# Kernel optimization log

Measured on AMD Instinct MI355X. Metric: run time of the kernel, lower is better.

The kernel has to match this reference:

```python
import jax, jax.numpy as jnp
import numpy as np
from jax import lax

RADIUS = 4
SIGMA_1 = 5.0
SIGMA_2 = 1.0


def _gaussian_kernel_3d(radius, sigma):
    x = np.linspace(-radius, radius, 2 * radius + 1)
    xx, yy, zz = np.meshgrid(x, x, x)
    dist2 = xx ** 2 + yy ** 2 + zz ** 2
    k = np.exp(-dist2 / (2.0 * sigma ** 2)).astype(np.float32)
    return jnp.asarray(k)[None, None]  # [O=1, I=1, D, H, W]


def _conv3d_same(x, kernel, radius):
    # x: [B,1,D,H,W], kernel: [1,1,kd,kh,kw]
    pad = [(radius, radius)] * 3
    return lax.conv_general_dilated(
        x, kernel, window_strides=(1, 1, 1), padding=pad,
        dimension_numbers=('NCDHW', 'OIDHW', 'NCDHW'))


def setup_inputs() -> dict:
    key = jax.random.key(0)
    k1, k2 = jax.random.split(key)
    labels = jax.random.uniform(k1, (4, 1, 160, 160, 160), dtype=jnp.float32)
    inputs = jax.random.uniform(k2, (4, 1, 160, 160, 160), dtype=jnp.float32)
    return {"labels": labels, "inputs": inputs}


def reference(labels, inputs):
    kernel = _gaussian_kernel_3d(RADIUS, SIGMA_1)
    num_classes = 2
    p0 = labels[:, 0:1]  # [B,1,D,H,W]
    loss = jnp.float32(0.0)
    for k in range(num_classes):
        class_probs = p0 if k == 0 else 1.0 - p0
        class_mean = (jnp.mean(inputs * class_probs, axis=(2, 3, 4), keepdims=True)
                      / (jnp.mean(class_probs, axis=(2, 3, 4), keepdims=True) + 1e-5))
        diff = jnp.sum((inputs - class_mean) ** 2, axis=1, keepdims=True)  # [B,1,D,H,W]
        weights = jnp.exp(-(diff ** 2) / (SIGMA_2 ** 2))
        numerator = jnp.sum(class_probs * _conv3d_same(class_probs * weights, kernel, RADIUS))
        denominator = jnp.sum(class_probs * _conv3d_same(weights, kernel, RADIUS))
        # L1Loss(scalar, 0) == abs(scalar)
        loss = loss + jnp.abs(numerator / (denominator + 1e-6))
    return jnp.float32(num_classes) - loss
```

## Files before the change

kernel.cpp:

```cpp
#include <hip/hip_runtime.h>
#include <hip/hip_fp16.h>
#include <math.h>

#define NX   160
#define N2   25600
#define N3   4096000
#define NB   4

#define ZPB  2
#define NBLK_XY 8000
#define BLKS_PER_B 2000

#define ZCH  10
#define NBLK_Z 1600

#define SB_W 36
#define SB_PLANE (40 * SB_W)

__device__ __constant__ float G1[9] = {
    0.72614903f, 0.83527021f, 0.92311635f, 0.98019867f, 1.0f,
    0.98019867f, 0.92311635f, 0.83527021f, 0.72614903f};

#define ES_FULL 7.92946852f
__device__ __constant__ float ES_M[4] = {3.46473426f, 2.48453559f, 1.56141924f,
                                         0.72614903f};
__device__ inline float edge_sum(int i) {
    float s = ES_FULL;
    if (i < 4) s -= ES_M[i];
    if (i > NX - 5) s -= ES_M[NX - 1 - i];
    return s;
}

__device__ inline float4 f4_zero() { return make_float4(0.f, 0.f, 0.f, 0.f); }
__device__ inline float4 f4_axpy(float a, float4 b, float4 c) {
    return make_float4(c.x + a * b.x, c.y + a * b.y, c.z + a * b.z, c.w + a * b.w);
}

__device__ inline float4 load_t4(const __half* p) {
    uint2 u = *(const uint2*)p;
    __half2 a = *(const __half2*)&u.x;
    __half2 b = *(const __half2*)&u.y;
    float2 fa = __half22float2(a);
    float2 fb = __half22float2(b);
    return make_float4(fa.x, fa.y, fb.x, fb.y);
}

template <int NV>
__device__ inline void block_reduce_store(double* vals, double* dst) {
    __shared__ double red[4][NV];
    int lane = threadIdx.x & 63;
    int wave = threadIdx.x >> 6;
#pragma unroll
    for (int v = 0; v < NV; ++v) {
        double x = vals[v];
#pragma unroll
        for (int off = 32; off > 0; off >>= 1) x += __shfl_down(x, off, 64);
        if (lane == 0) red[wave][v] = x;
    }
    __syncthreads();
    if (threadIdx.x < NV) {
        int v = threadIdx.x;
        dst[v] = red[0][v] + red[1][v] + red[2][v] + red[3][v];
    }
}

__global__ __launch_bounds__(256) void conv_xy_kernel(
    const float* __restrict__ labels, const float* __restrict__ inputs,
    __half* __restrict__ t, double* __restrict__ pS) {
    __shared__ float sB[ZPB * SB_PLANE];

    int bid = blockIdx.x;
    int tileX = bid % 5;
    int tileY = (bid / 5) % 5;
    int zq = (bid / 25) % 80;
    int b = bid / BLKS_PER_B;
    int zbase = zq * ZPB;
    int x0 = tileX * 32, y0 = tileY * 32;
    int tid = threadIdx.x;
    int baseOff = b * N3 + zbase * N2;

    for (int i = tid; i < ZPB * 320; i += 256) {
        int j = i / 320;
        int rem = i - 320 * j;
        int r = rem >> 3, x4 = rem & 7;
        int gy = y0 + r - 4;
        int gxf = x0 + 4 * x4 - 4;
        float w[12];
        if (gy >= 0 && gy < NX) {
            const float* row = &labels[baseOff + j * N2 + gy * NX];
#pragma unroll
            for (int c = 0; c < 3; ++c) {
                int gx = gxf + 4 * c;
                float4 v = (gx >= 0 && gx <= NX - 4) ? *(const float4*)&row[gx]
                                                     : f4_zero();
                w[4 * c] = v.x; w[4 * c + 1] = v.y;
                w[4 * c + 2] = v.z; w[4 * c + 3] = v.w;
            }
        } else {
#pragma unroll
            for (int c = 0; c < 12; ++c) w[c] = 0.f;
        }
        float4 o = f4_zero();
#pragma unroll
        for (int d = 0; d < 9; ++d) {
            float g = G1[d];
            o.x += g * w[d];
            o.y += g * w[d + 1];
            o.z += g * w[d + 2];
            o.w += g * w[d + 3];
        }
        *(float4*)&sB[j * SB_PLANE + r * SB_W + 4 * x4] = o;
    }
    __syncthreads();

    int oy = tid >> 3, x4 = tid & 7;
    double sp = 0.0, sip = 0.0, si = 0.0;
#pragma unroll
    for (int j = 0; j < ZPB; ++j) {
        float4 acc = f4_zero();
#pragma unroll
        for (int d = 0; d < 9; ++d) {
            float4 v = *(const float4*)&sB[j * SB_PLANE + (oy + d) * SB_W + 4 * x4];
            acc = f4_axpy(G1[d], v, acc);
        }
        int gi = baseOff + j * N2 + (y0 + oy) * NX + (x0 + 4 * x4);
        __half2 ha = __floats2half2_rn(acc.x, acc.y);
        __half2 hb = __floats2half2_rn(acc.z, acc.w);
        uint2 u;
        u.x = *(unsigned int*)&ha;
        u.y = *(unsigned int*)&hb;
        *(uint2*)&t[gi] = u;

        float4 p = *(const float4*)&labels[gi];
        float4 in = *(const float4*)&inputs[gi];
        sp += (double)(p.x + p.y + p.z + p.w);
        sip += (double)(in.x * p.x + in.y * p.y + in.z * p.z + in.w * p.w);
        si += (double)(in.x + in.y + in.z + in.w);
    }
    double vals[3] = {sp, sip, si};
    block_reduce_store<3>(vals, pS + 3 * bid);
}

__global__ __launch_bounds__(256) void reduce_S_kernel(
    const double* __restrict__ pS, double* __restrict__ S) {
    int b = blockIdx.x;
    double v0 = 0, v1 = 0, v2 = 0;
    for (int i = threadIdx.x; i < BLKS_PER_B; i += 256) {
        const double* p = pS + 3 * (b * BLKS_PER_B + i);
        v0 += p[0]; v1 += p[1]; v2 += p[2];
    }
    double vals[3] = {v0, v1, v2};
    block_reduce_store<3>(vals, S + 3 * b);
}

__global__ __launch_bounds__(256) void conv_z_kernel(
    const __half* __restrict__ t, const float* __restrict__ labels,
    const float* __restrict__ inputs, const double* __restrict__ S,
    double* __restrict__ pZ) {
    int tid = threadIdx.x;
    int tidg = blockIdx.x * 256 + tid;
    int x4 = tidg % 40;
    int r = tidg / 40;
    int y = r % NX;
    r /= NX;
    int zc = r % 16;
    int b = r / 16;

    double sp = S[3 * b + 0], sip = S[3 * b + 1], si = S[3 * b + 2];
    const double Nv = (double)N3;
    float m0 = (float)((sip / Nv) / (sp / Nv + 1e-5));
    float m1 = (float)(((si - sip) / Nv) / ((Nv - sp) / Nv + 1e-5));

    int x = x4 * 4;
    float ey = edge_sum(y);
    float cx[4] = {edge_sum(x) * ey, edge_sum(x + 1) * ey,
                   edge_sum(x + 2) * ey, edge_sum(x + 3) * ey};

    int z0 = zc * ZCH;
    int base = b * N3 + y * NX + x;

    float4 win[9];
#pragma unroll
    for (int d = 0; d < 9; ++d) {
        int z = z0 - 4 + d;
        win[d] = (z >= 0 && z < NX) ? load_t4(&t[base + z * N2]) : f4_zero();
    }

    float n0 = 0.f, d0 = 0.f, n1 = 0.f, d1 = 0.f;
    for (int zb = 0; zb < 5; ++zb) {
        int z = z0 + 2 * zb;
        float4 tn[2], pv[2], iv[2];
#pragma unroll
        for (int j = 0; j < 2; ++j) {
            int zl = z + j + 5;
            tn[j] = (zl < NX) ? load_t4(&t[base + zl * N2]) : f4_zero();
            int gi = base + (z + j) * N2;
            pv[j] = *(const float4*)&labels[gi];
            iv[j] = *(const float4*)&inputs[gi];
        }
#pragma unroll
        for (int j = 0; j < 2; ++j) {
            float4 c4 = f4_zero();
#pragma unroll
            for (int d = 0; d < 9; ++d) c4 = f4_axpy(G1[d], win[d], c4);
            float ez = edge_sum(z + j);
            float pc[4] = {pv[j].x, pv[j].y, pv[j].z, pv[j].w};
            float ic[4] = {iv[j].x, iv[j].y, iv[j].z, iv[j].w};
            float cc[4] = {c4.x, c4.y, c4.z, c4.w};
#pragma unroll
            for (int l = 0; l < 4; ++l) {
                float c1 = cx[l] * ez - cc[l];
                float df0 = ic[l] - m0; df0 *= df0;
                float w0 = __expf(-df0 * df0);
                float df1 = ic[l] - m1; df1 *= df1;
                float w1 = __expf(-df1 * df1);
                n0 += cc[l] * pc[l] * w0;
                d0 += cc[l] * w0;
                n1 += c1 * (1.f - pc[l]) * w1;
                d1 += c1 * w1;
            }
#pragma unroll
            for (int d = 0; d < 8; ++d) win[d] = win[d + 1];
            win[8] = tn[j];
        }
    }
    double vals[4] = {(double)n0, (double)d0, (double)n1, (double)d1};
    block_reduce_store<4>(vals, pZ + 4 * blockIdx.x);
}

__global__ __launch_bounds__(256) void finalize_kernel(
    const double* __restrict__ pZ, float* __restrict__ out) {
    double a0 = 0, a1 = 0, a2 = 0, a3 = 0;
    for (int i = threadIdx.x; i < NBLK_Z; i += 256) {
        const double* p = &pZ[4 * i];
        a0 += p[0]; a1 += p[1]; a2 += p[2]; a3 += p[3];
    }
    __shared__ double red[4][4];
    int lane = threadIdx.x & 63;
    int wave = threadIdx.x >> 6;
    double vals[4] = {a0, a1, a2, a3};
#pragma unroll
    for (int v = 0; v < 4; ++v) {
        double x = vals[v];
#pragma unroll
        for (int off = 32; off > 0; off >>= 1) x += __shfl_down(x, off, 64);
        if (lane == 0) red[wave][v] = x;
    }
    __syncthreads();
    if (threadIdx.x == 0) {
        double acc[4];
#pragma unroll
        for (int v = 0; v < 4; ++v)
            acc[v] = red[0][v] + red[1][v] + red[2][v] + red[3][v];
        double r0 = fabs(acc[0] / (acc[1] + 1e-6));
        double r1 = fabs(acc[2] / (acc[3] + 1e-6));
        out[0] = (float)(2.0 - r0 - r1);
    }
}

extern "C" void kernel_launch(void* const* d_in, const int* in_sizes, int n_in,
                              void* d_out, int out_size, void* d_ws, size_t ws_size,
                              hipStream_t stream) {
    const float* labels = (const float*)d_in[0];
    const float* inputs = (const float*)d_in[1];
    float* out = (float*)d_out;

    double* pS = (double*)d_ws;
    double* S  = (double*)((char*)d_ws + 192000);
    double* pZ = (double*)((char*)d_ws + 192128);
    __half* t  = (__half*)((char*)d_ws + 524288);

    hipLaunchKernelGGL(conv_xy_kernel, dim3(NBLK_XY), dim3(256), 0, stream,
                       labels, inputs, t, pS);
    hipLaunchKernelGGL(reduce_S_kernel, dim3(NB), dim3(256), 0, stream, pS, S);
    hipLaunchKernelGGL(conv_z_kernel, dim3(NBLK_Z), dim3(256), 0, stream,
                       t, labels, inputs, S, pZ);
    hipLaunchKernelGGL(finalize_kernel, dim3(1), dim3(256), 0, stream, pZ, out);
}
```

Baseline: 203.9 us.

## Fold per-batch mean reduction into conv_z and swizzle blocks across XCDs

Removes the separate reduce_S kernel launch. Every conv_z block now re-reduces the 2000 per-block partial sums for its batch and computes the class means locally. Block indices in both conv kernels are remapped so that consecutive logical tiles land on the same XCD, which is meant to improve L2 locality for neighbouring z-planes and halos. This saves one launch and its dependency gap, at the cost of each of the 1600 blocks redundantly reading 48KB of partials.

```diff
diff --git a/kernel.cpp b/kernel.cpp
--- a/kernel.cpp
+++ b/kernel.cpp
@@ -16,6 +16,10 @@
 
 #define SB_W 36
 #define SB_PLANE (40 * SB_W)
+
+__device__ inline int xcd_swz(int bid, int nblk) {
+    return (bid & 7) * (nblk >> 3) + (bid >> 3);
+}
 
 __device__ __constant__ float G1[9] = {
     0.72614903f, 0.83527021f, 0.92311635f, 0.98019867f, 1.0f,
@@ -69,7 +73,7 @@
     __half* __restrict__ t, double* __restrict__ pS) {
     __shared__ float sB[ZPB * SB_PLANE];
 
-    int bid = blockIdx.x;
+    int bid = xcd_swz(blockIdx.x, NBLK_XY);
     int tileX = bid % 5;
     int tileY = (bid / 5) % 5;
     int zq = (bid / 25) % 80;
@@ -141,24 +145,13 @@
     block_reduce_store<3>(vals, pS + 3 * bid);
 }
 
-__global__ __launch_bounds__(256) void reduce_S_kernel(
-    const double* __restrict__ pS, double* __restrict__ S) {
-    int b = blockIdx.x;
-    double v0 = 0, v1 = 0, v2 = 0;
-    for (int i = threadIdx.x; i < BLKS_PER_B; i += 256) {
-        const double* p = pS + 3 * (b * BLKS_PER_B + i);
-        v0 += p[0]; v1 += p[1]; v2 += p[2];
-    }
-    double vals[3] = {v0, v1, v2};
-    block_reduce_store<3>(vals, S + 3 * b);
-}
-
 __global__ __launch_bounds__(256) void conv_z_kernel(
     const __half* __restrict__ t, const float* __restrict__ labels,
-    const float* __restrict__ inputs, const double* __restrict__ S,
+    const float* __restrict__ inputs, const double* __restrict__ pS,
     double* __restrict__ pZ) {
     int tid = threadIdx.x;
-    int tidg = blockIdx.x * 256 + tid;
+    int lbid = xcd_swz(blockIdx.x, NBLK_Z);
+    int tidg = lbid * 256 + tid;
     int x4 = tidg % 40;
     int r = tidg / 40;
     int y = r % NX;
@@ -166,10 +159,35 @@
     int zc = r % 16;
     int b = r / 16;
 
-    double sp = S[3 * b + 0], sip = S[3 * b + 1], si = S[3 * b + 2];
-    const double Nv = (double)N3;
-    float m0 = (float)((sip / Nv) / (sp / Nv + 1e-5));
-    float m1 = (float)(((si - sip) / Nv) / ((Nv - sp) / Nv + 1e-5));
+    __shared__ float sM[2];
+    {
+        double v0 = 0, v1 = 0, v2 = 0;
+        for (int i = tid; i < BLKS_PER_B; i += 256) {
+            const double* p = pS + 3 * (b * BLKS_PER_B + i);
+            v0 += p[0]; v1 += p[1]; v2 += p[2];
+        }
+        __shared__ double red[4][3];
+        int lane = tid & 63, wave = tid >> 6;
+        double vals[3] = {v0, v1, v2};
+#pragma unroll
+        for (int v = 0; v < 3; ++v) {
+            double x = vals[v];
+#pragma unroll
+            for (int off = 32; off > 0; off >>= 1) x += __shfl_down(x, off, 64);
+            if (lane == 0) red[wave][v] = x;
+        }
+        __syncthreads();
+        if (tid == 0) {
+            double sp = red[0][0] + red[1][0] + red[2][0] + red[3][0];
+            double sip = red[0][1] + red[1][1] + red[2][1] + red[3][1];
+            double si = red[0][2] + red[1][2] + red[2][2] + red[3][2];
+            const double Nv = (double)N3;
+            sM[0] = (float)((sip / Nv) / (sp / Nv + 1e-5));
+            sM[1] = (float)(((si - sip) / Nv) / ((Nv - sp) / Nv + 1e-5));
+        }
+        __syncthreads();
+    }
+    float m0 = sM[0], m1 = sM[1];
 
     int x = x4 * 4;
     float ey = edge_sum(y);
@@ -225,7 +243,7 @@
         }
     }
     double vals[4] = {(double)n0, (double)d0, (double)n1, (double)d1};
-    block_reduce_store<4>(vals, pZ + 4 * blockIdx.x);
+    block_reduce_store<4>(vals, pZ + 4 * lbid);
 }
 
 __global__ __launch_bounds__(256) void finalize_kernel(
@@ -266,14 +284,12 @@
     float* out = (float*)d_out;
 
     double* pS = (double*)d_ws;
-    double* S  = (double*)((char*)d_ws + 192000);
     double* pZ = (double*)((char*)d_ws + 192128);
     __half* t  = (__half*)((char*)d_ws + 524288);
 
     hipLaunchKernelGGL(conv_xy_kernel, dim3(NBLK_XY), dim3(256), 0, stream,
                        labels, inputs, t, pS);
-    hipLaunchKernelGGL(reduce_S_kernel, dim3(NB), dim3(256), 0, stream, pS, S);
     hipLaunchKernelGGL(conv_z_kernel, dim3(NBLK_Z), dim3(256), 0, stream,
-                       t, labels, inputs, S, pZ);
+                       t, labels, inputs, pS, pZ);
     hipLaunchKernelGGL(finalize_kernel, dim3(1), dim3(256), 0, stream, pZ, out);
 }
```

New measurement: 202.2 us. About the same (-0.8%).
